# Kernel optimization log

Hardware: AMD Instinct MI355X
Metric: run time of the kernel (lower is better)

The kernel has to match this reference:

```python
import jax, jax.numpy as jnp
import numpy as np

_B, _T, _K, _P, _J, _D, _H = 8, 32, 8, 4, 24, 256, 8


def _layernorm(x, g, b, eps=1e-5):
    mu = jnp.mean(x, axis=-1, keepdims=True)
    var = jnp.mean(jnp.square(x - mu), axis=-1, keepdims=True)
    return (x - mu) * jax.lax.rsqrt(var + eps) * g + b


def setup_inputs() -> dict:
    key = jax.random.key(0)
    ks = jax.random.split(key, 12)
    D = _D
    p = lambda k, shape: jax.random.normal(k, shape, jnp.float32) * 0.02
    return {
        "pose_stream": jax.random.normal(ks[0], (_B, _T, _K, _P, _J, D), jnp.float32),
        "camera_stream": jax.random.normal(ks[1], (_B, _T, _K, D), jnp.float32),
        "ln1_g": jnp.ones((D,), jnp.float32),
        "ln1_b": jnp.zeros((D,), jnp.float32),
        "w_qkv1": p(ks[2], (3 * D, D)),
        "b_qkv1": p(ks[3], (3 * D,)),
        "w_o1": p(ks[4], (D, D)),
        "b_o1": p(ks[5], (D,)),
        "ln2_g": jnp.ones((D,), jnp.float32),
        "ln2_b": jnp.zeros((D,), jnp.float32),
        "w_qkv2": p(ks[6], (3 * D, D)),
        "b_qkv2": p(ks[7], (3 * D,)),
        "w_o2": p(ks[8], (D, D)),
        "b_o2": p(ks[9], (D,)),
        "B": _B, "T": _T, "K": _K, "P": _P, "J": _J, "D": _D,
    }


def reference(pose_stream, camera_stream, ln1_g, ln1_b, w_qkv1, b_qkv1, w_o1, b_o1,
              ln2_g, ln2_b, w_qkv2, b_qkv2, w_o2, b_o2, B, T, K, P, J, D):
    H = _H
    dh = D // H
    scale = 1.0 / np.sqrt(dh).astype(np.float32)

    # ---- Pose -> Camera: per (b,t,p,j), the K pose tokens attend to the K camera tokens ----
    wq1, wk1, wv1 = jnp.split(w_qkv1, 3, axis=0)
    bq1, bk1, bv1 = jnp.split(b_qkv1, 3, axis=0)
    qn = _layernorm(pose_stream, ln1_g, ln1_b)                      # (B,T,K,P,J,D)
    q = (qn @ wq1.T + bq1).reshape(B, T, K, P, J, H, dh)
    kc = (camera_stream @ wk1.T + bk1).reshape(B, T, K, H, dh)      # keys: camera tokens
    vc = (camera_stream @ wv1.T + bv1).reshape(B, T, K, H, dh)
    # scores over the camera axis k (keys); query axis is q (pose's own K index)
    s1 = jnp.einsum('btqpjhd,btkhd->btpjhqk', q, kc) * scale        # (B,T,P,J,H,K,K)
    a1 = jax.nn.softmax(s1, axis=-1)
    o1 = jnp.einsum('btpjhqk,btkhd->btqpjhd', a1, vc).reshape(B, T, K, P, J, D)
    o1 = o1 @ w_o1.T + b_o1
    pose_out = pose_stream + o1                                     # dropout p=0 -> identity

    # ---- Camera -> Pose: each camera token (query_len=1) attends to its P*J pose tokens ----
    wq2, wk2, wv2 = jnp.split(w_qkv2, 3, axis=0)
    bq2, bk2, bv2 = jnp.split(b_qkv2, 3, axis=0)
    cn = _layernorm(camera_stream, ln2_g, ln2_b)                    # (B,T,K,D)
    q2 = (cn @ wq2.T + bq2).reshape(B, T, K, H, dh)
    kv = pose_out.reshape(B, T, K, P * J, D)                        # keys/values from UPDATED pose
    k2 = (kv @ wk2.T + bk2).reshape(B, T, K, P * J, H, dh)
    v2 = (kv @ wv2.T + bv2).reshape(B, T, K, P * J, H, dh)
    s2 = jnp.einsum('btkhd,btknhd->btkhn', q2, k2) * scale          # (B,T,K,H,P*J)
    a2 = jax.nn.softmax(s2, axis=-1)
    o2 = jnp.einsum('btkhn,btknhd->btkhd', a2, v2).reshape(B, T, K, D)
    o2 = o2 @ w_o2.T + b_o2
    cam_out = camera_stream + o2
    return pose_out, cam_out
```

## Files before the change

kernel.cpp:

```cpp
#include <hip/hip_runtime.h>
#include <hip/hip_bf16.h>
#include <cstdint>
#include <cstddef>

#define SCALE1 0.17677669529663687f
#define POSE_ELEMS 50331648ll

typedef __attribute__((ext_vector_type(8))) short bf16x8;
typedef __attribute__((ext_vector_type(4))) float f32x4;

__device__ __forceinline__ unsigned short f2b(float f){
    unsigned int u = __float_as_uint(f);
    u = (u + 0x7FFFu + ((u >> 16) & 1u)) >> 16;
    return (unsigned short)u;
}
__device__ __forceinline__ float b2f(unsigned short s){
    return __uint_as_float(((unsigned int)s) << 16);
}
__device__ __forceinline__ float wredsum(float v){
    #pragma unroll
    for (int m = 1; m < 64; m <<= 1) v += __shfl_xor(v, m);
    return v;
}

__global__ __launch_bounds__(256) void k_conv2(
    const float* __restrict__ wqkv1, const float* __restrict__ wo1,
    const float* __restrict__ wqkv2, const float* __restrict__ wo2,
    unsigned short* __restrict__ wk1b,  unsigned short* __restrict__ wv1b,
    unsigned short* __restrict__ wq2b,  unsigned short* __restrict__ wq1Tb,
    unsigned short* __restrict__ wk2Tb, unsigned short* __restrict__ wo1b,
    unsigned short* __restrict__ wv2b,  unsigned short* __restrict__ wo2b)
{
    int t = blockIdx.x * 256 + threadIdx.x;
    int r = t >> 8, c = t & 255;
    wk1b[t] = f2b(wqkv1[(size_t)(256+r)*256 + c]);
    wv1b[t] = f2b(wqkv1[(size_t)(512+r)*256 + c]);
    wq2b[t] = f2b(wqkv2[t]);
    wo1b[t] = f2b(wo1[t]);
    wv2b[t] = f2b(wqkv2[(size_t)(512+r)*256 + c]);
    wo2b[t] = f2b(wo2[t]);
    wq1Tb[(size_t)c*256 + r] = f2b(wqkv1[t]);
    wk2Tb[(size_t)c*256 + r] = f2b(wqkv2[(size_t)(256+r)*256 + c]);
}

__global__ __launch_bounds__(512) void k_prep2(
    const float* __restrict__ cam, const float* __restrict__ ln2g, const float* __restrict__ ln2b,
    const float* __restrict__ bqkv1, const float* __restrict__ bqkv2,
    const unsigned short* __restrict__ wk1b,  const unsigned short* __restrict__ wv1b,
    const unsigned short* __restrict__ wq2b,  const unsigned short* __restrict__ wq1Tb,
    const unsigned short* __restrict__ wk2Tb, const unsigned short* __restrict__ wo1b,
    unsigned short* __restrict__ ckb, unsigned short* __restrict__ wv_oTb,
    unsigned short* __restrict__ uwb, float* __restrict__ cb1w)
{
    __shared__ __align__(16) unsigned short cln[2*4224];
    __shared__ __align__(16) unsigned short kcs [16*264];
    __shared__ __align__(16) unsigned short vcs [16*264];
    __shared__ __align__(16) unsigned short q2s [16*264];
    unsigned short* camb = cln;
    unsigned short* cnb  = cln + 4224;

    int tid = threadIdx.x;
    int wid = tid >> 6, lane = tid & 63;
    int fr = lane & 15, hi4 = lane >> 4, fk = hi4 * 8;
    int bt = blockIdx.x >> 1;
    int hf = blockIdx.x & 1;
    int r0 = bt * 8;

    {
        float4 g2v = ((const float4*)ln2g)[lane];
        float4 b2v = ((const float4*)ln2b)[lane];
        int row = wid;
        float4 f = ((const float4*)(cam + (size_t)(r0+row)*256))[lane];
        float s  = wredsum(f.x+f.y+f.z+f.w);
        float s2 = wredsum(f.x*f.x+f.y*f.y+f.z*f.z+f.w*f.w);
        float mu = s * (1.f/256.f);
        float rs = rsqrtf(s2*(1.f/256.f) - mu*mu + 1e-5f);
        ushort4 rawv, lnv;
        rawv.x = f2b(f.x); rawv.y = f2b(f.y); rawv.z = f2b(f.z); rawv.w = f2b(f.w);
        lnv.x = f2b((f.x-mu)*rs*g2v.x + b2v.x);
        lnv.y = f2b((f.y-mu)*rs*g2v.y + b2v.y);
        lnv.z = f2b((f.z-mu)*rs*g2v.z + b2v.z);
        lnv.w = f2b((f.w-mu)*rs*g2v.w + b2v.w);
        *(ushort4*)&camb[row*264 + lane*4] = rawv;
        *(ushort4*)&cnb [row*264 + lane*4] = lnv;
        for (int e = tid; e < 2112; e += 512){
            int off = 8*264 + e;
            camb[off] = 0; cnb[off] = 0; kcs[off] = 0; vcs[off] = 0; q2s[off] = 0;
        }
    }
    __syncthreads();

    for (int u = wid; u < 24; u += 8){
        int gm = u >> 3, nt = u & 7;
        const unsigned short* As = (gm == 2) ? cnb : camb;
        const unsigned short* Bw = (gm == 0) ? wk1b : (gm == 1) ? wv1b : wq2b;
        const float* bias = (gm == 0) ? (bqkv1 + 256) : (gm == 1) ? (bqkv1 + 512) : bqkv2;
        unsigned short* Dst = (gm == 0) ? kcs : (gm == 1) ? vcs : q2s;
        int col = hf*128 + nt*16 + fr;
        float bc = bias[col];
        f32x4 acc = (f32x4){0.f,0.f,0.f,0.f};
        for (int k0 = 0; k0 < 256; k0 += 32){
            bf16x8 a = *(const bf16x8*)&As[fr*264 + k0 + fk];
            bf16x8 b = *(const bf16x8*)&Bw[(size_t)col*256 + k0 + fk];
            acc = __builtin_amdgcn_mfma_f32_16x16x32_bf16(a, b, acc, 0, 0, 0);
        }
        if (hi4 < 2){
            #pragma unroll
            for (int i = 0; i < 4; i++)
                Dst[(hi4*4 + i)*264 + col] = f2b(acc[i] + bc);
        }
    }
    __syncthreads();

    if (tid < 32){
        int th = tid >> 3, kk = tid & 7;
        int h = hf*4 + th;
        float a = 0.f;
        for (int j = 0; j < 32; j++)
            a += bqkv1[h*32 + j] * b2f(kcs[kk*264 + h*32 + j]);
        cb1w[(size_t)bt*64 + h*8 + kk] = a;
    }

    unsigned short* stg = cln;
    for (int ot = 0; ot < 3; ot++){
        const unsigned short* As = (ot == 0) ? kcs : (ot == 1) ? q2s : vcs;
        const unsigned short* Bw = (ot == 0) ? wq1Tb : (ot == 1) ? wk2Tb : wo1b;
        __syncthreads();
        int hp = wid & 3;
        int h  = hf*4 + hp;
        int ntb = (wid >> 2) * 8;
        bf16x8 a = *(const bf16x8*)&As[fr*264 + h*32 + fk];
        for (int nt = ntb; nt < ntb + 8; nt++){
            int col = nt*16 + fr;
            bf16x8 b = *(const bf16x8*)&Bw[(size_t)col*256 + h*32 + fk];
            f32x4 acc = __builtin_amdgcn_mfma_f32_16x16x32_bf16(a, b, (f32x4){0.f,0.f,0.f,0.f}, 0, 0, 0);
            if (hi4 < 2){
                int kk0 = hi4*4;
                if (ot == 0){
                    #pragma unroll
                    for (int i = 0; i < 4; i++) stg[(hp*8 + kk0 + i)*256 + col] = f2b(acc[i]);
                } else if (ot == 1){
                    #pragma unroll
                    for (int i = 0; i < 4; i++) stg[(kk0 + i)*1024 + hp*256 + col] = f2b(acc[i]);
                } else {
                    ushort4 wv;
                    wv.x = f2b(acc[0]); wv.y = f2b(acc[1]); wv.z = f2b(acc[2]); wv.w = f2b(acc[3]);
                    *(ushort4*)&stg[col*32 + hp*8 + kk0] = wv;
                }
            }
        }
        __syncthreads();
        unsigned short* dst = (ot == 0) ? ckb : (ot == 1) ? uwb : wv_oTb;
        for (int cj = tid; cj < 1024; cj += 512){
            bf16x8 v = ((const bf16x8*)stg)[cj];
            size_t go;
            if (ot == 0){
                go = (size_t)bt*16384 + (size_t)hf*8192 + (size_t)cj*8;
            } else if (ot == 1){
                int r = cj >> 7, w = (cj*8) & 1023;
                go = (size_t)bt*16384 + (size_t)r*2048 + (size_t)hf*1024 + w;
            } else {
                int c = cj >> 2, v2 = (cj & 3)*8;
                go = (size_t)bt*16384 + (size_t)c*64 + (size_t)hf*32 + v2;
            }
            *(bf16x8*)(dst + go) = v;
        }
    }
}

__global__ __launch_bounds__(256) void k_pose(
    const float* __restrict__ pose,
    const float* __restrict__ ln1g, const float* __restrict__ ln1b,
    const float* __restrict__ bo1,
    const unsigned short* __restrict__ ckb, const unsigned short* __restrict__ wv_oTb,
    const float* __restrict__ cb1w, const unsigned short* __restrict__ uwb,
    float* __restrict__ out, unsigned short* __restrict__ ypw, float* __restrict__ yms)
{
    __shared__ __align__(16) unsigned short Xs[48*256];
    __shared__ __align__(16) unsigned short A1u[48*72];

    int tid = threadIdx.x;
    int bid = blockIdx.x;
    int g2 = (bid & 7) * 512 + (bid >> 3);
    int g = g2 >> 1, half = g2 & 1;
    int bt = g >> 3;
    int wid = tid >> 6, lane = tid & 63;
    int fr = lane & 15, hi4 = lane >> 4, fk = hi4 * 8;

    unsigned short (*A1)[72] = (unsigned short(*)[72])A1u;
    float (*sc)[48] = (float(*)[48])((char*)A1u + 2560);

    const float* pbase = pose + (size_t)g*96*256 + (size_t)half*48*256;
    float* obase = out + (size_t)g*96*256 + (size_t)half*48*256;

    int n1 = wid*16 + fr;
    const unsigned short* ckg = ckb + ((size_t)bt*64 + n1) * 256;
    float cb = cb1w[(size_t)bt*64 + n1];

    {
        float4 g1 = ((const float4*)ln1g)[lane];
        float4 b1 = ((const float4*)ln1b)[lane];
        #pragma unroll
        for (int rr = 0; rr < 12; rr++){
            int r = wid + rr*4;
            float4 f = ((const float4*)pbase)[(size_t)r * 64 + lane];
            float s  = wredsum(f.x+f.y+f.z+f.w);
            float s2 = wredsum(f.x*f.x+f.y*f.y+f.z*f.z+f.w*f.w);
            float mu = s * (1.f/256.f);
            float rs = rsqrtf(s2*(1.f/256.f) - mu*mu + 1e-5f);
            ushort4 qv;
            qv.x = f2b((f.x-mu)*rs*g1.x + b1.x);
            qv.y = f2b((f.y-mu)*rs*g1.y + b1.y);
            qv.z = f2b((f.z-mu)*rs*g1.z + b1.z);
            qv.w = f2b((f.w-mu)*rs*g1.w + b1.w);
            *(ushort4*)((char*)Xs + r*512 + ((lane*8) ^ ((r&7)<<4))) = qv;
        }
    }
    __syncthreads();

    {
        f32x4 acc[3];
        #pragma unroll
        for (int mt = 0; mt < 3; mt++) acc[mt] = (f32x4){0.f,0.f,0.f,0.f};
        #pragma unroll
        for (int kt = 0; kt < 8; kt++){
            int k0 = kt * 32;
            bf16x8 b = *(const bf16x8*)(ckg + k0 + fk);
            #pragma unroll
            for (int mt = 0; mt < 3; mt++){
                int r = mt*16 + fr;
                bf16x8 a = *(const bf16x8*)((char*)Xs + r*512 + (((k0+fk)*2) ^ ((r&7)<<4)));
                acc[mt] = __builtin_amdgcn_mfma_f32_16x16x32_bf16(a, b, acc[mt], 0, 0, 0);
            }
        }
        #pragma unroll
        for (int mt = 0; mt < 3; mt++){
            #pragma unroll
            for (int i = 0; i < 4; i++){
                float s = (acc[mt][i] + cb) * SCALE1;
                float mx = s;
                mx = fmaxf(mx, __shfl_xor(mx, 1));
                mx = fmaxf(mx, __shfl_xor(mx, 2));
                mx = fmaxf(mx, __shfl_xor(mx, 4));
                float e = __expf(s - mx);
                float sm = e;
                sm += __shfl_xor(sm, 1);
                sm += __shfl_xor(sm, 2);
                sm += __shfl_xor(sm, 4);
                A1[mt*16 + hi4*4 + i][n1] = f2b(e / sm);
            }
        }
    }
    __syncthreads();

    {
        const unsigned short* wvg = wv_oTb + (size_t)bt * 256 * 64;
        #pragma unroll
        for (int jt = 0; jt < 4; jt++){
            int col = wid*64 + jt*16 + fr;
            f32x4 acc2[3];
            #pragma unroll
            for (int mt = 0; mt < 3; mt++) acc2[mt] = (f32x4){0.f,0.f,0.f,0.f};
            #pragma unroll
            for (int k0 = 0; k0 < 64; k0 += 32){
                bf16x8 b = *(const bf16x8*)(wvg + (size_t)col*64 + k0 + fk);
                #pragma unroll
                for (int mt = 0; mt < 3; mt++){
                    bf16x8 a = *(const bf16x8*)&A1[mt*16 + fr][k0 + fk];
                    acc2[mt] = __builtin_amdgcn_mfma_f32_16x16x32_bf16(a, b, acc2[mt], 0, 0, 0);
                }
            }
            float bias = bo1[col];
            #pragma unroll
            for (int mt = 0; mt < 3; mt++)
                #pragma unroll
                for (int i = 0; i < 4; i++){
                    int row = mt*16 + hi4*4 + i;
                    *(unsigned short*)((char*)Xs + row*512 + ((col*2) ^ ((row&7)<<4))) = f2b(acc2[mt][i] + bias);
                }
        }
    }
    __syncthreads();

    {
        #pragma unroll
        for (int rr = 0; rr < 12; rr++){
            int r = wid + rr*4;
            float4 f = ((const float4*)pbase)[(size_t)r * 64 + lane];
            char* px = (char*)Xs + r*512 + ((lane*8) ^ ((r&7)<<4));
            ushort4 ov = *(ushort4*)px;
            float4 val;
            val.x = f.x + b2f(ov.x);
            val.y = f.y + b2f(ov.y);
            val.z = f.z + b2f(ov.z);
            val.w = f.w + b2f(ov.w);
            *(float4*)(obase + (size_t)r*256 + lane*4) = val;
            ushort4 nv;
            nv.x = f2b(val.x); nv.y = f2b(val.y); nv.z = f2b(val.z); nv.w = f2b(val.w);
            *(ushort4*)px = nv;
        }
    }
    __syncthreads();

    if (wid < 3){
        const unsigned short* ug = uwb + (size_t)g*2048;
        f32x4 a6 = (f32x4){0.f,0.f,0.f,0.f};
        for (int k0 = 0; k0 < 256; k0 += 32){
            bf16x8 u = *(const bf16x8*)(ug + (size_t)(fr & 7)*256 + k0 + fk);
            int r = wid*16 + fr;
            bf16x8 x = *(const bf16x8*)((char*)Xs + r*512 + (((k0+fk)*2) ^ ((r&7)<<4)));
            a6 = __builtin_amdgcn_mfma_f32_16x16x32_bf16(u, x, a6, 0, 0, 0);
        }
        if (hi4 < 2){
            #pragma unroll
            for (int i = 0; i < 4; i++)
                sc[hi4*4 + i][wid*16 + fr] = a6[i] * SCALE1;
        }
    }
    __syncthreads();

    unsigned short (*pb)[72] = (unsigned short(*)[72])A1u;
    if (wid == 0){
        int h = lane >> 3, j = lane & 7;
        float v[6];
        #pragma unroll
        for (int q = 0; q < 6; q++) v[q] = sc[h][j*6 + q];
        float mx = v[0];
        #pragma unroll
        for (int q = 1; q < 6; q++) mx = fmaxf(mx, v[q]);
        mx = fmaxf(mx, __shfl_xor(mx, 1));
        mx = fmaxf(mx, __shfl_xor(mx, 2));
        mx = fmaxf(mx, __shfl_xor(mx, 4));
        float e[6], s = 0.f;
        #pragma unroll
        for (int q = 0; q < 6; q++){ e[q] = __expf(v[q] - mx); s += e[q]; }
        s += __shfl_xor(s, 1);
        s += __shfl_xor(s, 2);
        s += __shfl_xor(s, 4);
        #pragma unroll
        for (int q = 0; q < 6; q++) pb[h][j*6 + q] = f2b(e[q]);
        if (j < 2){
            #pragma unroll
            for (int q = 0; q < 8; q++) pb[h][48 + j*8 + q] = 0;
        }
        if (j == 0){
            yms[(size_t)g2*16 + h*2]     = mx;
            yms[(size_t)g2*16 + h*2 + 1] = s;
        }
    }
    __syncthreads();

    unsigned short* ystg = (unsigned short*)((char*)A1u + 2560);
    {
        #pragma unroll
        for (int nth = 0; nth < 2; nth++){
            f32x4 ay[2];
            ay[0] = (f32x4){0.f,0.f,0.f,0.f};
            ay[1] = (f32x4){0.f,0.f,0.f,0.f};
            #pragma unroll
            for (int k0 = 0; k0 < 64; k0 += 32){
                bf16x8 a8 = *(const bf16x8*)&pb[fr][k0 + fk];
                #pragma unroll
                for (int nt = 0; nt < 2; nt++){
                    int col = wid*64 + (nth*2+nt)*16 + fr;
                    union { bf16x8 v; unsigned short u[8]; } bx;
                    #pragma unroll
                    for (int jj = 0; jj < 8; jj++){
                        int rr = k0 + fk + jj;
                        rr = (rr < 48) ? rr : 47;
                        bx.u[jj] = *(const unsigned short*)((char*)Xs + rr*512 + ((col*2) ^ ((rr&7)<<4)));
                    }
                    ay[nt] = __builtin_amdgcn_mfma_f32_16x16x32_bf16(a8, bx.v, ay[nt], 0, 0, 0);
                }
            }
            if (hi4 < 2){
                #pragma unroll
                for (int nt = 0; nt < 2; nt++)
                    #pragma unroll
                    for (int i = 0; i < 4; i++)
                        ystg[(hi4*4 + i)*256 + wid*64 + (nth*2+nt)*16 + fr] = f2b(ay[nt][i]);
            }
        }
    }
    __syncthreads();
    ((bf16x8*)(ypw + (size_t)g2*2048))[tid] = ((const bf16x8*)ystg)[tid];
}

__global__ __launch_bounds__(512) void k_cam2(
    const float* __restrict__ cam,
    const float* __restrict__ bqkv2, const float* __restrict__ bo2,
    const unsigned short* __restrict__ wv2b, const unsigned short* __restrict__ wo2b,
    const unsigned short* __restrict__ ypw, const float* __restrict__ yms,
    float* __restrict__ out)
{
    __shared__ __align__(16) unsigned short ycb[8][16][264];
    __shared__ __align__(16) unsigned short o2s[16][264];
    __shared__ __align__(16) float wf[8][8][2];

    int tid = threadIdx.x;
    int bt = blockIdx.x;
    int wid = tid >> 6, lane = tid & 63;
    int fr = lane & 15, hi4 = lane >> 4, fk = hi4 * 8;

    for (int e = tid; e < 16896; e += 512)
        ((unsigned short*)ycb)[(e/2112)*16*264 + (8 + (e%2112)/264)*264 + (e%264)] = 0;
    for (int e = tid; e < 2112; e += 512) o2s[8 + e/264][e%264] = 0;

    if (tid < 64){
        int gl = tid >> 3, h = tid & 7;
        const float* ms0 = yms + (size_t)(bt*16 + gl*2)*16 + h*2;
        float m0 = ms0[0], s0 = ms0[1];
        float m1 = ms0[16], s1 = ms0[17];
        float m = fmaxf(m0, m1);
        float w0 = __expf(m0 - m), w1 = __expf(m1 - m);
        float inv = 1.f / (s0*w0 + s1*w1);
        wf[gl][h][0] = w0*inv; wf[gl][h][1] = w1*inv;
    }
    __syncthreads();

    for (int e = tid; e < 2048; e += 512){
        int gl = e >> 8, rest = e & 255, h = rest >> 5, i8 = rest & 31;
        const unsigned short* y0 = ypw + (size_t)(bt*16 + gl*2)*2048 + h*256 + i8*8;
        bf16x8 v0 = *(const bf16x8*)y0;
        bf16x8 v1 = *(const bf16x8*)(y0 + 2048);
        float f0 = wf[gl][h][0], f1 = wf[gl][h][1];
        union { bf16x8 v; unsigned short u[8]; } rr;
        #pragma unroll
        for (int q = 0; q < 8; q++)
            rr.u[q] = f2b(b2f((unsigned short)v0[q])*f0 + b2f((unsigned short)v1[q])*f1);
        *(bf16x8*)&ycb[h][gl][i8*8] = rr.v;
    }
    __syncthreads();

    for (int u = wid; u < 16; u += 8){
        int h = u >> 1, nt = u & 1;
        int m = h*32 + nt*16 + fr;
        f32x4 acc = (f32x4){0.f,0.f,0.f,0.f};
        for (int k0 = 0; k0 < 256; k0 += 32){
            bf16x8 a = *(const bf16x8*)&ycb[h][fr][k0 + fk];
            bf16x8 b = *(const bf16x8*)(wv2b + (size_t)m*256 + k0 + fk);
            acc = __builtin_amdgcn_mfma_f32_16x16x32_bf16(a, b, acc, 0, 0, 0);
        }
        if (hi4 < 2){
            float bv = bqkv2[512 + m];
            #pragma unroll
            for (int i = 0; i < 4; i++)
                o2s[hi4*4 + i][m] = f2b(acc[i] + bv);
        }
    }
    __syncthreads();

    const float* camg = cam + (size_t)bt*8*256;
    float* og = out + POSE_ELEMS + (size_t)bt*8*256;
    for (int u = wid; u < 16; u += 8){
        int col = u*16 + fr;
        f32x4 acc = (f32x4){0.f,0.f,0.f,0.f};
        for (int k0 = 0; k0 < 256; k0 += 32){
            bf16x8 a = *(const bf16x8*)&o2s[fr][k0 + fk];
            bf16x8 b = *(const bf16x8*)(wo2b + (size_t)col*256 + k0 + fk);
            acc = __builtin_amdgcn_mfma_f32_16x16x32_bf16(a, b, acc, 0, 0, 0);
        }
        if (hi4 < 2){
            float bc = bo2[col];
            #pragma unroll
            for (int i = 0; i < 4; i++){
                int gg = hi4*4 + i;
                og[(size_t)gg*256 + col] = acc[i] + bc + camg[(size_t)gg*256 + col];
            }
        }
    }
}

extern "C" void kernel_launch(void* const* d_in, const int* in_sizes, int n_in,
                              void* d_out, int out_size, void* d_ws, size_t ws_size,
                              hipStream_t stream)
{
    const float* pose  = (const float*)d_in[0];
    const float* camr  = (const float*)d_in[1];
    const float* ln1g  = (const float*)d_in[2];
    const float* ln1b  = (const float*)d_in[3];
    const float* wqkv1 = (const float*)d_in[4];
    const float* bqkv1 = (const float*)d_in[5];
    const float* wo1   = (const float*)d_in[6];
    const float* bo1   = (const float*)d_in[7];
    const float* ln2g  = (const float*)d_in[8];
    const float* ln2b  = (const float*)d_in[9];
    const float* wqkv2 = (const float*)d_in[10];
    const float* bqkv2 = (const float*)d_in[11];
    const float* wo2   = (const float*)d_in[12];
    const float* bo2   = (const float*)d_in[13];
    float* out = (float*)d_out;
    char* ws = (char*)d_ws;

    size_t off = 0;
    unsigned short* ckb    = (unsigned short*)(ws + off); off += 8388608;
    unsigned short* wv_oTb = (unsigned short*)(ws + off); off += 8388608;
    unsigned short* uwb    = (unsigned short*)(ws + off); off += 8388608 + 8192;
    unsigned short* ypw    = (unsigned short*)(ws + off); off += 16777216;
    float*          yms    = (float*)(ws + off);          off += 262144;
    unsigned short* wts    = (unsigned short*)(ws + off); off += 8*131072;
    unsigned short* wk1b  = wts;
    unsigned short* wv1b  = wts + 1*65536;
    unsigned short* wq2b  = wts + 2*65536;
    unsigned short* wq1Tb = wts + 3*65536;
    unsigned short* wk2Tb = wts + 4*65536;
    unsigned short* wo1b  = wts + 5*65536;
    unsigned short* wv2b  = wts + 6*65536;
    unsigned short* wo2b  = wts + 7*65536;
    float* cb1w = (float*)(ws + off);                      off += 65536;

    k_conv2<<<dim3(256), dim3(256), 0, stream>>>(wqkv1, wo1, wqkv2, wo2,
                                                 wk1b, wv1b, wq2b, wq1Tb, wk2Tb, wo1b, wv2b, wo2b);
    k_prep2<<<dim3(512), dim3(512), 0, stream>>>(camr, ln2g, ln2b, bqkv1, bqkv2,
                                                 wk1b, wv1b, wq2b, wq1Tb, wk2Tb, wo1b,
                                                 ckb, wv_oTb, uwb, cb1w);
    k_pose<<<dim3(4096), dim3(256), 0, stream>>>(pose, ln1g, ln1b, bo1,
                                                 ckb, wv_oTb, cb1w, uwb, out, ypw, yms);
    k_cam2<<<dim3(256), dim3(512), 0, stream>>>(camr, bqkv2, bo2, wv2b, wo2b, ypw, yms, out);
}
```

Measured before the change: 181.5 us.

## Split each pose group into three 32-row blocks instead of two 48-row blocks

The pose kernel now processes 32 rows per block instead of 48, launching 6144 blocks instead of 4096. This shrinks LDS per block and removes the padded/clamped K dimension in the P·X MFMA, likely raising occupancy. The partial softmax statistics and outputs are now merged from three partitions in the camera kernel. The cost is more blocks, more partial-result traffic and more redundant per-block loads of ckb and weights.

```diff
diff --git a/kernel.cpp b/kernel.cpp
--- a/kernel.cpp
+++ b/kernel.cpp
@@ -176,22 +176,24 @@
     const float* __restrict__ cb1w, const unsigned short* __restrict__ uwb,
     float* __restrict__ out, unsigned short* __restrict__ ypw, float* __restrict__ yms)
 {
-    __shared__ __align__(16) unsigned short Xs[48*256];
-    __shared__ __align__(16) unsigned short A1u[48*72];
+    __shared__ __align__(16) unsigned short Xs[32*256];
+    __shared__ __align__(16) unsigned short A1u[2688];
 
     int tid = threadIdx.x;
     int bid = blockIdx.x;
-    int g2 = (bid & 7) * 512 + (bid >> 3);
-    int g = g2 >> 1, half = g2 & 1;
+    int g3 = (bid & 7) * 768 + (bid >> 3);
+    int g = g3 / 3, part = g3 - g*3;
     int bt = g >> 3;
     int wid = tid >> 6, lane = tid & 63;
     int fr = lane & 15, hi4 = lane >> 4, fk = hi4 * 8;
 
     unsigned short (*A1)[72] = (unsigned short(*)[72])A1u;
-    float (*sc)[48] = (float(*)[48])((char*)A1u + 2560);
-
-    const float* pbase = pose + (size_t)g*96*256 + (size_t)half*48*256;
-    float* obase = out + (size_t)g*96*256 + (size_t)half*48*256;
+    unsigned short (*pb)[40] = (unsigned short(*)[40])A1u;
+    float (*sc)[32] = (float(*)[32])((char*)A1u + 1280);
+    unsigned short* ystg = (unsigned short*)((char*)A1u + 2304);
+
+    const float* pbase = pose + (size_t)g*96*256 + (size_t)part*32*256;
+    float* obase = out + (size_t)g*96*256 + (size_t)part*32*256;
 
     int n1 = wid*16 + fr;
     const unsigned short* ckg = ckb + ((size_t)bt*64 + n1) * 256;
@@ -201,7 +203,7 @@
         float4 g1 = ((const float4*)ln1g)[lane];
         float4 b1 = ((const float4*)ln1b)[lane];
         #pragma unroll
-        for (int rr = 0; rr < 12; rr++){
+        for (int rr = 0; rr < 8; rr++){
             int r = wid + rr*4;
             float4 f = ((const float4*)pbase)[(size_t)r * 64 + lane];
             float s  = wredsum(f.x+f.y+f.z+f.w);
@@ -219,22 +221,22 @@
     __syncthreads();
 
     {
-        f32x4 acc[3];
-        #pragma unroll
-        for (int mt = 0; mt < 3; mt++) acc[mt] = (f32x4){0.f,0.f,0.f,0.f};
+        f32x4 acc[2];
+        acc[0] = (f32x4){0.f,0.f,0.f,0.f};
+        acc[1] = (f32x4){0.f,0.f,0.f,0.f};
         #pragma unroll
         for (int kt = 0; kt < 8; kt++){
             int k0 = kt * 32;
             bf16x8 b = *(const bf16x8*)(ckg + k0 + fk);
             #pragma unroll
-            for (int mt = 0; mt < 3; mt++){
+            for (int mt = 0; mt < 2; mt++){
                 int r = mt*16 + fr;
                 bf16x8 a = *(const bf16x8*)((char*)Xs + r*512 + (((k0+fk)*2) ^ ((r&7)<<4)));
                 acc[mt] = __builtin_amdgcn_mfma_f32_16x16x32_bf16(a, b, acc[mt], 0, 0, 0);
             }
         }
         #pragma unroll
-        for (int mt = 0; mt < 3; mt++){
+        for (int mt = 0; mt < 2; mt++){
             #pragma unroll
             for (int i = 0; i < 4; i++){
                 float s = (acc[mt][i] + cb) * SCALE1;
@@ -258,21 +260,21 @@
         #pragma unroll
         for (int jt = 0; jt < 4; jt++){
             int col = wid*64 + jt*16 + fr;
-            f32x4 acc2[3];
-            #pragma unroll
-            for (int mt = 0; mt < 3; mt++) acc2[mt] = (f32x4){0.f,0.f,0.f,0.f};
+            f32x4 acc2[2];
+            acc2[0] = (f32x4){0.f,0.f,0.f,0.f};
+            acc2[1] = (f32x4){0.f,0.f,0.f,0.f};
             #pragma unroll
             for (int k0 = 0; k0 < 64; k0 += 32){
                 bf16x8 b = *(const bf16x8*)(wvg + (size_t)col*64 + k0 + fk);
                 #pragma unroll
-                for (int mt = 0; mt < 3; mt++){
+                for (int mt = 0; mt < 2; mt++){
                     bf16x8 a = *(const bf16x8*)&A1[mt*16 + fr][k0 + fk];
                     acc2[mt] = __builtin_amdgcn_mfma_f32_16x16x32_bf16(a, b, acc2[mt], 0, 0, 0);
                 }
             }
             float bias = bo1[col];
             #pragma unroll
-            for (int mt = 0; mt < 3; mt++)
+            for (int mt = 0; mt < 2; mt++)
                 #pragma unroll
                 for (int i = 0; i < 4; i++){
                     int row = mt*16 + hi4*4 + i;
@@ -284,7 +286,7 @@
 
     {
         #pragma unroll
-        for (int rr = 0; rr < 12; rr++){
+        for (int rr = 0; rr < 8; rr++){
             int r = wid + rr*4;
             float4 f = ((const float4*)pbase)[(size_t)r * 64 + lane];
             char* px = (char*)Xs + r*512 + ((lane*8) ^ ((r&7)<<4));
@@ -302,7 +304,7 @@
     }
     __syncthreads();
 
-    if (wid < 3){
+    if (wid < 2){
         const unsigned short* ug = uwb + (size_t)g*2048;
         f32x4 a6 = (f32x4){0.f,0.f,0.f,0.f};
         for (int k0 = 0; k0 < 256; k0 += 32){
@@ -319,59 +321,47 @@
     }
     __syncthreads();
 
-    unsigned short (*pb)[72] = (unsigned short(*)[72])A1u;
     if (wid == 0){
         int h = lane >> 3, j = lane & 7;
-        float v[6];
-        #pragma unroll
-        for (int q = 0; q < 6; q++) v[q] = sc[h][j*6 + q];
-        float mx = v[0];
-        #pragma unroll
-        for (int q = 1; q < 6; q++) mx = fmaxf(mx, v[q]);
+        float v[4];
+        #pragma unroll
+        for (int q = 0; q < 4; q++) v[q] = sc[h][j*4 + q];
+        float mx = fmaxf(fmaxf(v[0], v[1]), fmaxf(v[2], v[3]));
         mx = fmaxf(mx, __shfl_xor(mx, 1));
         mx = fmaxf(mx, __shfl_xor(mx, 2));
         mx = fmaxf(mx, __shfl_xor(mx, 4));
-        float e[6], s = 0.f;
-        #pragma unroll
-        for (int q = 0; q < 6; q++){ e[q] = __expf(v[q] - mx); s += e[q]; }
+        float e[4], s = 0.f;
+        #pragma unroll
+        for (int q = 0; q < 4; q++){ e[q] = __expf(v[q] - mx); s += e[q]; }
         s += __shfl_xor(s, 1);
         s += __shfl_xor(s, 2);
         s += __shfl_xor(s, 4);
         #pragma unroll
-        for (int q = 0; q < 6; q++) pb[h][j*6 + q] = f2b(e[q]);
-        if (j < 2){
-            #pragma unroll
-            for (int q = 0; q < 8; q++) pb[h][48 + j*8 + q] = 0;
-        }
+        for (int q = 0; q < 4; q++) pb[h][j*4 + q] = f2b(e[q]);
         if (j == 0){
-            yms[(size_t)g2*16 + h*2]     = mx;
-            yms[(size_t)g2*16 + h*2 + 1] = s;
-        }
-    }
-    __syncthreads();
-
-    unsigned short* ystg = (unsigned short*)((char*)A1u + 2560);
+            yms[(size_t)g3*16 + h*2]     = mx;
+            yms[(size_t)g3*16 + h*2 + 1] = s;
+        }
+    }
+    __syncthreads();
+
     {
+        bf16x8 a8 = *(const bf16x8*)&pb[fr][fk];
         #pragma unroll
         for (int nth = 0; nth < 2; nth++){
             f32x4 ay[2];
             ay[0] = (f32x4){0.f,0.f,0.f,0.f};
             ay[1] = (f32x4){0.f,0.f,0.f,0.f};
             #pragma unroll
-            for (int k0 = 0; k0 < 64; k0 += 32){
-                bf16x8 a8 = *(const bf16x8*)&pb[fr][k0 + fk];
+            for (int nt = 0; nt < 2; nt++){
+                int col = wid*64 + (nth*2+nt)*16 + fr;
+                union { bf16x8 v; unsigned short u[8]; } bx;
                 #pragma unroll
-                for (int nt = 0; nt < 2; nt++){
-                    int col = wid*64 + (nth*2+nt)*16 + fr;
-                    union { bf16x8 v; unsigned short u[8]; } bx;
-                    #pragma unroll
-                    for (int jj = 0; jj < 8; jj++){
-                        int rr = k0 + fk + jj;
-                        rr = (rr < 48) ? rr : 47;
-                        bx.u[jj] = *(const unsigned short*)((char*)Xs + rr*512 + ((col*2) ^ ((rr&7)<<4)));
-                    }
-                    ay[nt] = __builtin_amdgcn_mfma_f32_16x16x32_bf16(a8, bx.v, ay[nt], 0, 0, 0);
+                for (int jj = 0; jj < 8; jj++){
+                    int rr = fk + jj;
+                    bx.u[jj] = *(const unsigned short*)((char*)Xs + rr*512 + ((col*2) ^ ((rr&7)<<4)));
                 }
+                ay[nt] = __builtin_amdgcn_mfma_f32_16x16x32_bf16(a8, bx.v, ay[nt], 0, 0, 0);
             }
             if (hi4 < 2){
                 #pragma unroll
@@ -383,7 +373,7 @@
         }
     }
     __syncthreads();
-    ((bf16x8*)(ypw + (size_t)g2*2048))[tid] = ((const bf16x8*)ystg)[tid];
+    ((bf16x8*)(ypw + (size_t)g3*2048))[tid] = ((const bf16x8*)ystg)[tid];
 }
 
 __global__ __launch_bounds__(512) void k_cam2(
@@ -395,7 +385,7 @@
 {
     __shared__ __align__(16) unsigned short ycb[8][16][264];
     __shared__ __align__(16) unsigned short o2s[16][264];
-    __shared__ __align__(16) float wf[8][8][2];
+    __shared__ __align__(16) float wf[8][8][3];
 
     int tid = threadIdx.x;
     int bt = blockIdx.x;
@@ -408,26 +398,29 @@
 
     if (tid < 64){
         int gl = tid >> 3, h = tid & 7;
-        const float* ms0 = yms + (size_t)(bt*16 + gl*2)*16 + h*2;
-        float m0 = ms0[0], s0 = ms0[1];
-        float m1 = ms0[16], s1 = ms0[17];
-        float m = fmaxf(m0, m1);
-        float w0 = __expf(m0 - m), w1 = __expf(m1 - m);
-        float inv = 1.f / (s0*w0 + s1*w1);
-        wf[gl][h][0] = w0*inv; wf[gl][h][1] = w1*inv;
+        size_t g3b = ((size_t)(bt*8 + gl)) * 3;
+        float m0 = yms[(g3b+0)*16 + h*2],     s0 = yms[(g3b+0)*16 + h*2 + 1];
+        float m1 = yms[(g3b+1)*16 + h*2],     s1 = yms[(g3b+1)*16 + h*2 + 1];
+        float m2 = yms[(g3b+2)*16 + h*2],     s2 = yms[(g3b+2)*16 + h*2 + 1];
+        float m = fmaxf(fmaxf(m0, m1), m2);
+        float w0 = __expf(m0 - m), w1 = __expf(m1 - m), w2 = __expf(m2 - m);
+        float inv = 1.f / (s0*w0 + s1*w1 + s2*w2);
+        wf[gl][h][0] = w0*inv; wf[gl][h][1] = w1*inv; wf[gl][h][2] = w2*inv;
     }
     __syncthreads();
 
     for (int e = tid; e < 2048; e += 512){
         int gl = e >> 8, rest = e & 255, h = rest >> 5, i8 = rest & 31;
-        const unsigned short* y0 = ypw + (size_t)(bt*16 + gl*2)*2048 + h*256 + i8*8;
+        const unsigned short* y0 = ypw + ((size_t)(bt*8 + gl)*3)*2048 + h*256 + i8*8;
         bf16x8 v0 = *(const bf16x8*)y0;
         bf16x8 v1 = *(const bf16x8*)(y0 + 2048);
-        float f0 = wf[gl][h][0], f1 = wf[gl][h][1];
+        bf16x8 v2 = *(const bf16x8*)(y0 + 4096);
+        float f0 = wf[gl][h][0], f1 = wf[gl][h][1], f2 = wf[gl][h][2];
         union { bf16x8 v; unsigned short u[8]; } rr;
         #pragma unroll
         for (int q = 0; q < 8; q++)
-            rr.u[q] = f2b(b2f((unsigned short)v0[q])*f0 + b2f((unsigned short)v1[q])*f1);
+            rr.u[q] = f2b(b2f((unsigned short)v0[q])*f0 + b2f((unsigned short)v1[q])*f1
+                        + b2f((unsigned short)v2[q])*f2);
         *(bf16x8*)&ycb[h][gl][i8*8] = rr.v;
     }
     __syncthreads();
@@ -496,8 +489,8 @@
     unsigned short* ckb    = (unsigned short*)(ws + off); off += 8388608;
     unsigned short* wv_oTb = (unsigned short*)(ws + off); off += 8388608;
     unsigned short* uwb    = (unsigned short*)(ws + off); off += 8388608 + 8192;
-    unsigned short* ypw    = (unsigned short*)(ws + off); off += 16777216;
-    float*          yms    = (float*)(ws + off);          off += 262144;
+    unsigned short* ypw    = (unsigned short*)(ws + off); off += 25165824;
+    float*          yms    = (float*)(ws + off);          off += 393216;
     unsigned short* wts    = (unsigned short*)(ws + off); off += 8*131072;
     unsigned short* wk1b  = wts;
     unsigned short* wv1b  = wts + 1*65536;
@@ -514,7 +507,7 @@
     k_prep2<<<dim3(512), dim3(512), 0, stream>>>(camr, ln2g, ln2b, bqkv1, bqkv2,
                                                  wk1b, wv1b, wq2b, wq1Tb, wk2Tb, wo1b,
                                                  ckb, wv_oTb, uwb, cb1w);
-    k_pose<<<dim3(4096), dim3(256), 0, stream>>>(pose, ln1g, ln1b, bo1,
+    k_pose<<<dim3(6144), dim3(256), 0, stream>>>(pose, ln1g, ln1b, bo1,
                                                  ckb, wv_oTb, cb1w, uwb, out, ypw, yms);
     k_cam2<<<dim3(256), dim3(512), 0, stream>>>(camr, bqkv2, bo2, wv2b, wo2b, ypw, yms, out);
 }
```

After: 189.9 us. 4.6% more time.
